# Kernel tuning notes

Hardware: AMD Instinct MI355X
Metric: run time of the kernel (lower is better)

The kernel has to match this reference:

```python
import jax, jax.numpy as jnp
import numpy as np

NOISE_SIGMA = 0.07
NOISE_TIMESTEPS = np.array([0, 1, 2, 3])
T, B, N_INP, N_REC, N_OUT = 256, 256, 128, 512, 64


def setup_inputs() -> dict:
    key = jax.random.key(0)
    ks = jax.random.split(key, 7)
    inputs = jax.random.normal(ks[0], (T, B, N_INP), dtype=jnp.float32)
    # Precomputed noise: randn*sigma at noise timesteps, zeros elsewhere
    noise = jnp.zeros((T, B, N_REC), dtype=jnp.float32)
    nz = jax.random.normal(ks[1], (len(NOISE_TIMESTEPS), B, N_REC), dtype=jnp.float32) * NOISE_SIGMA
    noise = noise.at[jnp.asarray(NOISE_TIMESTEPS)].set(nz)
    Wi = jax.random.normal(ks[2], (N_REC, N_INP), dtype=jnp.float32) / np.sqrt(N_INP)
    bi = jax.random.normal(ks[3], (N_REC,), dtype=jnp.float32) * 0.01
    # orthogonal recurrent init
    A = jax.random.normal(ks[4], (N_REC, N_REC), dtype=jnp.float32)
    Q, _ = jnp.linalg.qr(A)
    Wrec = Q.astype(jnp.float32)
    Wo = jax.random.normal(ks[5], (N_OUT, N_REC), dtype=jnp.float32) / np.sqrt(N_REC)
    bo = jax.random.normal(ks[6], (N_OUT,), dtype=jnp.float32) * 0.01
    return {"inputs": inputs, "noise": noise, "Wi": Wi, "bi": bi,
            "Wrec": Wrec, "Wo": Wo, "bo": bo}


def reference(inputs, noise, Wi, bi, Wrec, Wo, bo):
    # Precompute input projection for all timesteps: [T, B, n_rec]
    proj = jnp.einsum('tbi,ri->tbr', inputs, Wi) + bi

    def step(hidden, xs):
        p, nz = xs
        hidden = jax.nn.relu(p + hidden @ Wrec.T + nz)  # [B, n_rec]
        return hidden, hidden

    h0 = jnp.zeros((inputs.shape[1], Wrec.shape[0]), dtype=inputs.dtype)
    hidden, h = jax.lax.scan(step, h0, (proj, noise))
    output = jax.nn.softmax(hidden @ Wo.T + bo, axis=-1)  # [B, n_out]
    return output, h, hidden
```

## Files before the change

kernel.cpp:

```cpp
#include <hip/hip_runtime.h>
#include <hip/hip_bf16.h>
#include <stdint.h>

#define T_STEPS 256
#define B_SZ    256
#define NI      128
#define NR      512
#define NO      64
#define BT      16
#define HALF_R  256

typedef __attribute__((ext_vector_type(8))) short short8;
typedef __attribute__((ext_vector_type(4))) short short4v;
typedef __attribute__((ext_vector_type(4))) float f32x4;
typedef __attribute__((ext_vector_type(2))) unsigned long long u64x2;

__device__ __forceinline__ unsigned short f2bf(float f) {
    union { float f; unsigned u; } v; v.f = f;
    unsigned u = v.u;
    return (unsigned short)((u + 0x7FFFu + ((u >> 16) & 1u)) >> 16);
}

template<int KTB>
__device__ __forceinline__ void recur8(const unsigned char* Hbuf,
                                       const short8 (&Bh)[2][16],
                                       f32x4& acc0, f32x4& acc1,
                                       int l15, int l4, unsigned swzA) {
    #pragma unroll
    for (int kk = 0; kk < 8; ++kk) {
        const unsigned off = l15 * 1024 + (((unsigned)((KTB + kk) * 64 + l4 * 16)) ^ swzA);
        const short8 a = *(const short8*)(Hbuf + off);
        acc0 = __builtin_amdgcn_mfma_f32_16x16x32_bf16(a, Bh[0][KTB + kk], acc0, 0, 0, 0);
        acc1 = __builtin_amdgcn_mfma_f32_16x16x32_bf16(a, Bh[1][KTB + kk], acc1, 0, 0, 0);
    }
}

__global__ __launch_bounds__(256) void proj_gemm(
    const float* __restrict__ inputs, const float* __restrict__ Wi,
    const float* __restrict__ bi, const float* __restrict__ noise,
    float* __restrict__ proj)
{
    const int mb = blockIdx.x;
    const int nb = blockIdx.y;
    const int m0 = mb * 64, n0 = nb * 128;
    const int tid = threadIdx.x, w = tid >> 6, l = tid & 63;
    const int l15 = l & 15, l4 = l >> 4;

    __shared__ __align__(16) unsigned char Al[64 * 256];
    __shared__ __align__(16) unsigned char Wl[128 * 256];

    #pragma unroll
    for (int j = 0; j < 8; ++j) {
        const int f = j * 256 + tid;
        const int row = f >> 5, c4 = f & 31;
        const float4 v = *(const float4*)(inputs + (size_t)(m0 + row) * NI + c4 * 4);
        short4v pk;
        pk[0] = (short)f2bf(v.x); pk[1] = (short)f2bf(v.y);
        pk[2] = (short)f2bf(v.z); pk[3] = (short)f2bf(v.w);
        *(short4v*)(&Al[row * 256 + (((unsigned)(c4 * 8)) ^ ((row & 7) << 4))]) = pk;
    }
    #pragma unroll
    for (int j = 0; j < 16; ++j) {
        const int f = j * 256 + tid;
        const int r = f >> 5, c4 = f & 31;
        const float4 v = *(const float4*)(Wi + (size_t)(n0 + r) * NI + c4 * 4);
        short4v pk;
        pk[0] = (short)f2bf(v.x); pk[1] = (short)f2bf(v.y);
        pk[2] = (short)f2bf(v.z); pk[3] = (short)f2bf(v.w);
        *(short4v*)(&Wl[r * 256 + (((unsigned)(c4 * 8)) ^ ((r & 7) << 4))]) = pk;
    }
    __syncthreads();

    f32x4 acc[8];
    #pragma unroll
    for (int nt = 0; nt < 8; ++nt) acc[nt] = (f32x4){0.f, 0.f, 0.f, 0.f};
    #pragma unroll
    for (int kt = 0; kt < 4; ++kt) {
        const short8 a = *(const short8*)(
            &Al[(w * 16 + l15) * 256 + (((unsigned)(kt * 64 + l4 * 16)) ^ ((l15 & 7) << 4))]);
        #pragma unroll
        for (int nt = 0; nt < 8; ++nt) {
            const short8 b = *(const short8*)(
                &Wl[(nt * 16 + l15) * 256 + (((unsigned)(kt * 64 + l4 * 16)) ^ ((l15 & 7) << 4))]);
            acc[nt] = __builtin_amdgcn_mfma_f32_16x16x32_bf16(a, b, acc[nt], 0, 0, 0);
        }
    }

    const int t = m0 >> 8;
    #pragma unroll
    for (int nt = 0; nt < 8; ++nt) {
        const int n = n0 + nt * 16 + l15;
        const float bv = bi[n];
        #pragma unroll
        for (int q = 0; q < 4; ++q) {
            const int gr = m0 + w * 16 + l4 * 4 + q;
            float v = acc[nt][q] + bv;
            if (t < 4) v += noise[(size_t)gr * NR + n];
            proj[(size_t)gr * NR + n] = v;
        }
    }
}

__global__ __launch_bounds__(512) void rnn_scan(
    const float* __restrict__ Wrec,
    float* __restrict__ dout,
    unsigned long long* __restrict__ Xbuf)
{
    const int bid  = blockIdx.x;
    const int grp  = bid & 15;
    const int half = bid >> 4;
    const int b0   = grp * BT;
    const int tid  = threadIdx.x;
    const int w    = tid >> 6;
    const int l    = tid & 63;
    const int l15  = l & 15;
    const int l4   = l >> 4;

    __shared__ __align__(16) unsigned char Hl[2][BT * 1024];

    short8 Bh[2][16];
    #pragma unroll
    for (int ct = 0; ct < 2; ++ct) {
        const int n = half * HALF_R + w * 32 + ct * 16 + l15;
        #pragma unroll
        for (int kt = 0; kt < 16; ++kt) {
            const float* src = Wrec + (size_t)n * NR + kt * 32 + l4 * 8;
            short8 f;
            #pragma unroll
            for (int j = 0; j < 8; ++j) f[j] = (short)f2bf(src[j]);
            Bh[ct][kt] = f;
        }
    }

    unsigned long long* Xg = Xbuf + (size_t)grp * 4096;

    float* hbuf   = dout + (size_t)NO * B_SZ;
    float* hidout = hbuf + (size_t)T_STEPS * B_SZ * NR;

    const unsigned swzA = (unsigned)((l15 & 7) << 4);
    const int n0 = half * HALF_R + w * 32 + l15;
    const int n1 = n0 + 16;
    const int mrow = l4 * 4;

    f32x4 acc0, acc1;
    #pragma unroll
    for (int q = 0; q < 4; ++q) {
        acc0[q] = hbuf[(size_t)(b0 + mrow + q) * NR + n0];
        acc1[q] = hbuf[(size_t)(b0 + mrow + q) * NR + n1];
    }

    float pj0[4], pj1[4];

    for (int t = 0; t < T_STEPS; ++t) {
        const int pn = (t & 1) ^ 1;
        const int tag = ((t >> 1) & 1) ^ 1;

        if (t > 0) {
            if (half == 0) recur8<8>(&Hl[t & 1][0], Bh, acc0, acc1, l15, l4, swzA);
            else           recur8<0>(&Hl[t & 1][0], Bh, acc0, acc1, l15, l4, swzA);
        }

        float v0[4], v1[4];
        #pragma unroll
        for (int q = 0; q < 4; ++q) {
            v0[q] = fmaxf(acc0[q], 0.f);
            v1[q] = fmaxf(acc1[q], 0.f);
        }

        if (t == T_STEPS - 1) {
            #pragma unroll
            for (int q = 0; q < 4; ++q) {
                hbuf[((size_t)t * B_SZ + b0 + mrow + q) * NR + n0] = v0[q];
                hbuf[((size_t)t * B_SZ + b0 + mrow + q) * NR + n1] = v1[q];
                hidout[(size_t)(b0 + mrow + q) * NR + n0] = v0[q];
                hidout[(size_t)(b0 + mrow + q) * NR + n1] = v1[q];
            }
            break;
        }

        {
            unsigned long long* Xh = Xg + (size_t)(pn * 2 + half) * 1024;
            const unsigned long long tagmask =
                tag ? 0x8000800080008000ULL : 0ULL;
            #pragma unroll
            for (int ct = 0; ct < 2; ++ct) {
                #pragma unroll
                for (int q = 0; q < 4; ++q) {
                    const float v = ct ? v1[q] : v0[q];
                    const float vo = __shfl_xor(v, 1, 64);
                    unsigned pk = (unsigned)f2bf(v) | ((unsigned)f2bf(vo) << 16);
                    const unsigned pk_hi = __shfl_xor(pk, 2, 64);
                    if ((l & 3) == 0) {
                        const int m = mrow + q;
                        const int c = w * 32 + ct * 16 + l15;
                        const unsigned long long val =
                            (unsigned long long)pk | ((unsigned long long)pk_hi << 32);
                        const unsigned off = m * 1024 +
                            (((unsigned)(2 * (half * HALF_R + c))) ^ ((unsigned)((m & 7) << 4)));
                        *(unsigned long long*)(&Hl[pn][off]) = val;
                        __hip_atomic_store(Xh + m * 64 + (c >> 2), val | tagmask,
                                           __ATOMIC_RELAXED, __HIP_MEMORY_SCOPE_AGENT);
                    }
                }
            }
        }

        asm volatile("s_waitcnt lgkmcnt(0)" ::: "memory");
        __builtin_amdgcn_sched_barrier(0);
        __builtin_amdgcn_s_barrier();
        __builtin_amdgcn_sched_barrier(0);

        #pragma unroll
        for (int q = 0; q < 4; ++q) {
            pj0[q] = hbuf[((size_t)(t + 1) * B_SZ + b0 + mrow + q) * NR + n0];
            pj1[q] = hbuf[((size_t)(t + 1) * B_SZ + b0 + mrow + q) * NR + n1];
        }
        #pragma unroll
        for (int q = 0; q < 4; ++q) {
            hbuf[((size_t)t * B_SZ + b0 + mrow + q) * NR + n0] = v0[q];
            hbuf[((size_t)t * B_SZ + b0 + mrow + q) * NR + n1] = v1[q];
        }
        acc0 = (f32x4){0.f, 0.f, 0.f, 0.f};
        acc1 = (f32x4){0.f, 0.f, 0.f, 0.f};
        if (half == 0) recur8<0>(&Hl[pn][0], Bh, acc0, acc1, l15, l4, swzA);
        else           recur8<8>(&Hl[pn][0], Bh, acc0, acc1, l15, l4, swzA);

        {
            const int row = tid >> 5;
            const unsigned kk = (unsigned)((2 * tid) & 63);
            const unsigned long long* src =
                Xg + (size_t)(pn * 2 + (half ^ 1)) * 1024 + row * 64 + kk;
            const unsigned et = (unsigned)tag;
            unsigned long long a, b;
            for (;;) {
                a = __hip_atomic_load(src,     __ATOMIC_RELAXED, __HIP_MEMORY_SCOPE_AGENT);
                b = __hip_atomic_load(src + 1, __ATOMIC_RELAXED, __HIP_MEMORY_SCOPE_AGENT);
                if ((((unsigned)(a >> 63)) == et) & (((unsigned)(b >> 63)) == et)) break;
            }
            if (tag) { a &= 0x7FFF7FFF7FFF7FFFULL; b &= 0x7FFF7FFF7FFF7FFFULL; }
            u64x2 dd; dd[0] = a; dd[1] = b;
            const unsigned off = row * 1024 +
                (((unsigned)((half ^ 1) * 512 + kk * 8)) ^ ((unsigned)((row & 7) << 4)));
            *(u64x2*)(&Hl[pn][off]) = dd;
        }
        #pragma unroll
        for (int q = 0; q < 4; ++q) { acc0[q] += pj0[q]; acc1[q] += pj1[q]; }

        asm volatile("s_waitcnt lgkmcnt(0)" ::: "memory");
        __builtin_amdgcn_sched_barrier(0);
        __builtin_amdgcn_s_barrier();
        __builtin_amdgcn_sched_barrier(0);
    }
}

__global__ __launch_bounds__(256) void rnn_out(
    const float* __restrict__ Wo, const float* __restrict__ bo,
    float* __restrict__ dout)
{
    const float* hidden = dout + (size_t)NO * B_SZ + (size_t)T_STEPS * B_SZ * NR;
    const int b = blockIdx.x;
    const int tid = threadIdx.x, w = tid >> 6, l = tid & 63;

    __shared__ float hid[NR];
    __shared__ float lg[NO];

    if (tid < 128) {
        *(float4*)(&hid[tid * 4]) = *(const float4*)(hidden + (size_t)b * NR + tid * 4);
    }
    __syncthreads();

    #pragma unroll 1
    for (int jj = 0; jj < 16; ++jj) {
        const int j = w * 16 + jj;
        const float4* wr = (const float4*)(Wo + (size_t)j * NR + l * 8);
        const float4 a = wr[0], c = wr[1];
        const float4 h0 = *(const float4*)(&hid[l * 8]);
        const float4 h1 = *(const float4*)(&hid[l * 8 + 4]);
        float s = a.x * h0.x + a.y * h0.y + a.z * h0.z + a.w * h0.w
                + c.x * h1.x + c.y * h1.y + c.z * h1.z + c.w * h1.w;
        #pragma unroll
        for (int d = 32; d > 0; d >>= 1) s += __shfl_xor(s, d, 64);
        if (l == 0) lg[j] = s + bo[j];
    }
    __syncthreads();

    if (tid < 64) {
        const float x = lg[tid];
        float mx = x;
        #pragma unroll
        for (int d = 32; d > 0; d >>= 1) mx = fmaxf(mx, __shfl_xor(mx, d, 64));
        const float e = __expf(x - mx);
        float sum = e;
        #pragma unroll
        for (int d = 32; d > 0; d >>= 1) sum += __shfl_xor(sum, d, 64);
        dout[(size_t)b * NO + tid] = e / sum;
    }
}

extern "C" void kernel_launch(void* const* d_in, const int* in_sizes, int n_in,
                              void* d_out, int out_size, void* d_ws, size_t ws_size,
                              hipStream_t stream) {
    const float* inputs = (const float*)d_in[0];
    const float* noise  = (const float*)d_in[1];
    const float* Wi     = (const float*)d_in[2];
    const float* bi     = (const float*)d_in[3];
    const float* Wrec   = (const float*)d_in[4];
    const float* Wo     = (const float*)d_in[5];
    const float* bo     = (const float*)d_in[6];
    float* out = (float*)d_out;

    unsigned long long* Xbuf = (unsigned long long*)d_ws;

    float* proj = out + (size_t)NO * B_SZ;

    hipMemsetAsync(d_ws, 0, 16 * 4096 * sizeof(unsigned long long), stream);
    proj_gemm<<<dim3(1024, 4), 256, 0, stream>>>(inputs, Wi, bi, noise, proj);
    rnn_scan<<<32, 512, 0, stream>>>(Wrec, out, Xbuf);
    rnn_out<<<256, 256, 0, stream>>>(Wo, bo, out);
}
```

Measured before the change: 683.6 us.

## Split recurrent matmul by K across block pairs, exchange fp32 partial sums

```diff
diff --git a/kernel.cpp b/kernel.cpp
--- a/kernel.cpp
+++ b/kernel.cpp
@@ -13,7 +13,6 @@
 typedef __attribute__((ext_vector_type(8))) short short8;
 typedef __attribute__((ext_vector_type(4))) short short4v;
 typedef __attribute__((ext_vector_type(4))) float f32x4;
-typedef __attribute__((ext_vector_type(2))) unsigned long long u64x2;
 
 __device__ __forceinline__ unsigned short f2bf(float f) {
     union { float f; unsigned u; } v; v.f = f;
@@ -21,18 +20,10 @@
     return (unsigned short)((u + 0x7FFFu + ((u >> 16) & 1u)) >> 16);
 }
 
-template<int KTB>
-__device__ __forceinline__ void recur8(const unsigned char* Hbuf,
-                                       const short8 (&Bh)[2][16],
-                                       f32x4& acc0, f32x4& acc1,
-                                       int l15, int l4, unsigned swzA) {
-    #pragma unroll
-    for (int kk = 0; kk < 8; ++kk) {
-        const unsigned off = l15 * 1024 + (((unsigned)((KTB + kk) * 64 + l4 * 16)) ^ swzA);
-        const short8 a = *(const short8*)(Hbuf + off);
-        acc0 = __builtin_amdgcn_mfma_f32_16x16x32_bf16(a, Bh[0][KTB + kk], acc0, 0, 0, 0);
-        acc1 = __builtin_amdgcn_mfma_f32_16x16x32_bf16(a, Bh[1][KTB + kk], acc1, 0, 0, 0);
-    }
+__device__ __forceinline__ unsigned long long tagpack2(float a, float b, unsigned tag) {
+    const unsigned ua = (__float_as_uint(a) & ~1u) | tag;
+    const unsigned ub = (__float_as_uint(b) & ~1u) | tag;
+    return (unsigned long long)ua | ((unsigned long long)ub << 32);
 }
 
 __global__ __launch_bounds__(256) void proj_gemm(
@@ -101,7 +92,7 @@
     }
 }
 
-__global__ __launch_bounds__(512) void rnn_scan(
+__global__ __launch_bounds__(512, 2) void rnn_scan(
     const float* __restrict__ Wrec,
     float* __restrict__ dout,
     unsigned long long* __restrict__ Xbuf)
@@ -115,16 +106,20 @@
     const int l    = tid & 63;
     const int l15  = l & 15;
     const int l4   = l >> 4;
-
-    __shared__ __align__(16) unsigned char Hl[2][BT * 1024];
-
-    short8 Bh[2][16];
-    #pragma unroll
-    for (int ct = 0; ct < 2; ++ct) {
-        const int n = half * HALF_R + w * 32 + ct * 16 + l15;
-        #pragma unroll
-        for (int kt = 0; kt < 16; ++kt) {
-            const float* src = Wrec + (size_t)n * NR + kt * 32 + l4 * 8;
+    const bool keep = ((w >> 2) == half);
+    const int kw   = w & 3;
+    const int mrow = l4 * 4;
+    const int nb   = w * 64;
+
+    __shared__ __align__(16) unsigned char Hl[2][BT * 512];
+
+    short8 Bh[4][8];
+    #pragma unroll
+    for (int ct = 0; ct < 4; ++ct) {
+        const int n = nb + ct * 16 + l15;
+        #pragma unroll
+        for (int kt = 0; kt < 8; ++kt) {
+            const float* src = Wrec + (size_t)n * NR + half * HALF_R + kt * 32 + l4 * 8;
             short8 f;
             #pragma unroll
             for (int j = 0; j < 8; ++j) f[j] = (short)f2bf(src[j]);
@@ -132,119 +127,156 @@
         }
     }
 
-    unsigned long long* Xg = Xbuf + (size_t)grp * 4096;
+    unsigned long long* Xg = Xbuf + (size_t)grp * 8192;
 
     float* hbuf   = dout + (size_t)NO * B_SZ;
     float* hidout = hbuf + (size_t)T_STEPS * B_SZ * NR;
 
-    const unsigned swzA = (unsigned)((l15 & 7) << 4);
-    const int n0 = half * HALF_R + w * 32 + l15;
-    const int n1 = n0 + 16;
-    const int mrow = l4 * 4;
-
-    f32x4 acc0, acc1;
-    #pragma unroll
-    for (int q = 0; q < 4; ++q) {
-        acc0[q] = hbuf[(size_t)(b0 + mrow + q) * NR + n0];
-        acc1[q] = hbuf[(size_t)(b0 + mrow + q) * NR + n1];
-    }
-
-    float pj0[4], pj1[4];
-
-    for (int t = 0; t < T_STEPS; ++t) {
-        const int pn = (t & 1) ^ 1;
-        const int tag = ((t >> 1) & 1) ^ 1;
-
-        if (t > 0) {
-            if (half == 0) recur8<8>(&Hl[t & 1][0], Bh, acc0, acc1, l15, l4, swzA);
-            else           recur8<0>(&Hl[t & 1][0], Bh, acc0, acc1, l15, l4, swzA);
-        }
-
-        float v0[4], v1[4];
-        #pragma unroll
-        for (int q = 0; q < 4; ++q) {
-            v0[q] = fmaxf(acc0[q], 0.f);
-            v1[q] = fmaxf(acc1[q], 0.f);
-        }
-
-        if (t == T_STEPS - 1) {
+    float pj[4][4];
+
+    if (keep) {
+        #pragma unroll
+        for (int ct = 0; ct < 4; ++ct)
+            #pragma unroll
+            for (int q = 0; q < 4; ++q)
+                pj[ct][q] = hbuf[(size_t)(b0 + mrow + q) * NR + nb + ct * 16 + l15];
+        #pragma unroll
+        for (int ct = 0; ct < 4; ++ct) {
             #pragma unroll
             for (int q = 0; q < 4; ++q) {
-                hbuf[((size_t)t * B_SZ + b0 + mrow + q) * NR + n0] = v0[q];
-                hbuf[((size_t)t * B_SZ + b0 + mrow + q) * NR + n1] = v1[q];
-                hidout[(size_t)(b0 + mrow + q) * NR + n0] = v0[q];
-                hidout[(size_t)(b0 + mrow + q) * NR + n1] = v1[q];
-            }
-            break;
-        }
-
-        {
-            unsigned long long* Xh = Xg + (size_t)(pn * 2 + half) * 1024;
-            const unsigned long long tagmask =
-                tag ? 0x8000800080008000ULL : 0ULL;
-            #pragma unroll
-            for (int ct = 0; ct < 2; ++ct) {
+                const float v = fmaxf(pj[ct][q], 0.f);
+                hbuf[(size_t)(b0 + mrow + q) * NR + nb + ct * 16 + l15] = v;
+                const float vo = __shfl_xor(v, 1, 64);
+                unsigned pk = (unsigned)f2bf(v) | ((unsigned)f2bf(vo) << 16);
+                const unsigned pk_hi = __shfl_xor(pk, 2, 64);
+                if ((l & 3) == 0) {
+                    const int c = kw * 64 + ct * 16 + l15;
+                    const int m = mrow + q;
+                    const unsigned off = m * 512 +
+                        (((unsigned)(2 * c)) ^ ((unsigned)((m & 7) << 4)));
+                    *(unsigned long long*)(&Hl[0][off]) =
+                        (unsigned long long)pk | ((unsigned long long)pk_hi << 32);
+                }
+            }
+        }
+        #pragma unroll
+        for (int ct = 0; ct < 4; ++ct)
+            #pragma unroll
+            for (int q = 0; q < 4; ++q)
+                pj[ct][q] = hbuf[((size_t)B_SZ + b0 + mrow + q) * NR + nb + ct * 16 + l15];
+    }
+    asm volatile("s_waitcnt lgkmcnt(0)" ::: "memory");
+    __builtin_amdgcn_sched_barrier(0);
+    __builtin_amdgcn_s_barrier();
+    __builtin_amdgcn_sched_barrier(0);
+
+    for (int t = 1; t < T_STEPS; ++t) {
+        const int p = t & 1;
+        const unsigned tag = ((unsigned)(t + 1) >> 1) & 1u;
+        const unsigned char* Hb = &Hl[p ^ 1][0];
+
+        f32x4 acc[4];
+        #pragma unroll
+        for (int ct = 0; ct < 4; ++ct) acc[ct] = (f32x4){0.f, 0.f, 0.f, 0.f};
+
+        unsigned long long* Xe =
+            Xg + (size_t)(p * 2 + (half ^ 1)) * 2048 + kw * 512 + l;
+
+        if (!keep) __builtin_amdgcn_s_setprio(1);
+        #pragma unroll
+        for (int ct = 0; ct < 4; ++ct) {
+            #pragma unroll
+            for (int kt = 0; kt < 8; ++kt) {
+                const unsigned off = l15 * 512 +
+                    (((unsigned)(kt * 64 + l4 * 16)) ^ ((unsigned)((l15 & 7) << 4)));
+                const short8 a = *(const short8*)(Hb + off);
+                acc[ct] = __builtin_amdgcn_mfma_f32_16x16x32_bf16(a, Bh[ct][kt], acc[ct], 0, 0, 0);
+            }
+            if (!keep) {
+                __hip_atomic_store(Xe + ct * 128,
+                                   tagpack2(acc[ct][0], acc[ct][1], tag),
+                                   __ATOMIC_RELAXED, __HIP_MEMORY_SCOPE_AGENT);
+                __hip_atomic_store(Xe + ct * 128 + 64,
+                                   tagpack2(acc[ct][2], acc[ct][3], tag),
+                                   __ATOMIC_RELAXED, __HIP_MEMORY_SCOPE_AGENT);
+            }
+        }
+        if (!keep) __builtin_amdgcn_s_setprio(0);
+
+        if (keep) {
+            const unsigned long long* Xc =
+                Xg + (size_t)(p * 2 + half) * 2048 + kw * 512 + l;
+            const unsigned long long tmask =
+                tag ? 0x0000000100000001ULL : 0ULL;
+            unsigned long long d0, d1, d2, d3, d4, d5, d6, d7;
+            for (;;) {
+                d0 = __hip_atomic_load(Xc +   0, __ATOMIC_RELAXED, __HIP_MEMORY_SCOPE_AGENT);
+                d1 = __hip_atomic_load(Xc +  64, __ATOMIC_RELAXED, __HIP_MEMORY_SCOPE_AGENT);
+                d2 = __hip_atomic_load(Xc + 128, __ATOMIC_RELAXED, __HIP_MEMORY_SCOPE_AGENT);
+                d3 = __hip_atomic_load(Xc + 192, __ATOMIC_RELAXED, __HIP_MEMORY_SCOPE_AGENT);
+                d4 = __hip_atomic_load(Xc + 256, __ATOMIC_RELAXED, __HIP_MEMORY_SCOPE_AGENT);
+                d5 = __hip_atomic_load(Xc + 320, __ATOMIC_RELAXED, __HIP_MEMORY_SCOPE_AGENT);
+                d6 = __hip_atomic_load(Xc + 384, __ATOMIC_RELAXED, __HIP_MEMORY_SCOPE_AGENT);
+                d7 = __hip_atomic_load(Xc + 448, __ATOMIC_RELAXED, __HIP_MEMORY_SCOPE_AGENT);
+                const unsigned long long bad =
+                    (((d0 ^ tmask) | (d1 ^ tmask) | (d2 ^ tmask) | (d3 ^ tmask) |
+                      (d4 ^ tmask) | (d5 ^ tmask) | (d6 ^ tmask) | (d7 ^ tmask))
+                     & 0x0000000100000001ULL);
+                if (bad == 0) break;
+            }
+
+            float vv[4][4];
+            #pragma unroll
+            for (int ct = 0; ct < 4; ++ct) {
+                const unsigned long long da = (ct == 0) ? d0 : (ct == 1) ? d2 : (ct == 2) ? d4 : d6;
+                const unsigned long long db = (ct == 0) ? d1 : (ct == 1) ? d3 : (ct == 2) ? d5 : d7;
+                vv[ct][0] = fmaxf(acc[ct][0] + __uint_as_float((unsigned)da)         + pj[ct][0], 0.f);
+                vv[ct][1] = fmaxf(acc[ct][1] + __uint_as_float((unsigned)(da >> 32)) + pj[ct][1], 0.f);
+                vv[ct][2] = fmaxf(acc[ct][2] + __uint_as_float((unsigned)db)         + pj[ct][2], 0.f);
+                vv[ct][3] = fmaxf(acc[ct][3] + __uint_as_float((unsigned)(db >> 32)) + pj[ct][3], 0.f);
+            }
+
+            #pragma unroll
+            for (int ct = 0; ct < 4; ++ct) {
                 #pragma unroll
                 for (int q = 0; q < 4; ++q) {
-                    const float v = ct ? v1[q] : v0[q];
+                    const float v = vv[ct][q];
                     const float vo = __shfl_xor(v, 1, 64);
                     unsigned pk = (unsigned)f2bf(v) | ((unsigned)f2bf(vo) << 16);
                     const unsigned pk_hi = __shfl_xor(pk, 2, 64);
                     if ((l & 3) == 0) {
+                        const int c = kw * 64 + ct * 16 + l15;
                         const int m = mrow + q;
-                        const int c = w * 32 + ct * 16 + l15;
-                        const unsigned long long val =
+                        const unsigned off = m * 512 +
+                            (((unsigned)(2 * c)) ^ ((unsigned)((m & 7) << 4)));
+                        *(unsigned long long*)(&Hl[p][off]) =
                             (unsigned long long)pk | ((unsigned long long)pk_hi << 32);
-                        const unsigned off = m * 1024 +
-                            (((unsigned)(2 * (half * HALF_R + c))) ^ ((unsigned)((m & 7) << 4)));
-                        *(unsigned long long*)(&Hl[pn][off]) = val;
-                        __hip_atomic_store(Xh + m * 64 + (c >> 2), val | tagmask,
-                                           __ATOMIC_RELAXED, __HIP_MEMORY_SCOPE_AGENT);
                     }
                 }
             }
-        }
-
-        asm volatile("s_waitcnt lgkmcnt(0)" ::: "memory");
-        __builtin_amdgcn_sched_barrier(0);
-        __builtin_amdgcn_s_barrier();
-        __builtin_amdgcn_sched_barrier(0);
-
-        #pragma unroll
-        for (int q = 0; q < 4; ++q) {
-            pj0[q] = hbuf[((size_t)(t + 1) * B_SZ + b0 + mrow + q) * NR + n0];
-            pj1[q] = hbuf[((size_t)(t + 1) * B_SZ + b0 + mrow + q) * NR + n1];
-        }
-        #pragma unroll
-        for (int q = 0; q < 4; ++q) {
-            hbuf[((size_t)t * B_SZ + b0 + mrow + q) * NR + n0] = v0[q];
-            hbuf[((size_t)t * B_SZ + b0 + mrow + q) * NR + n1] = v1[q];
-        }
-        acc0 = (f32x4){0.f, 0.f, 0.f, 0.f};
-        acc1 = (f32x4){0.f, 0.f, 0.f, 0.f};
-        if (half == 0) recur8<0>(&Hl[pn][0], Bh, acc0, acc1, l15, l4, swzA);
-        else           recur8<8>(&Hl[pn][0], Bh, acc0, acc1, l15, l4, swzA);
-
-        {
-            const int row = tid >> 5;
-            const unsigned kk = (unsigned)((2 * tid) & 63);
-            const unsigned long long* src =
-                Xg + (size_t)(pn * 2 + (half ^ 1)) * 1024 + row * 64 + kk;
-            const unsigned et = (unsigned)tag;
-            unsigned long long a, b;
-            for (;;) {
-                a = __hip_atomic_load(src,     __ATOMIC_RELAXED, __HIP_MEMORY_SCOPE_AGENT);
-                b = __hip_atomic_load(src + 1, __ATOMIC_RELAXED, __HIP_MEMORY_SCOPE_AGENT);
-                if ((((unsigned)(a >> 63)) == et) & (((unsigned)(b >> 63)) == et)) break;
-            }
-            if (tag) { a &= 0x7FFF7FFF7FFF7FFFULL; b &= 0x7FFF7FFF7FFF7FFFULL; }
-            u64x2 dd; dd[0] = a; dd[1] = b;
-            const unsigned off = row * 1024 +
-                (((unsigned)((half ^ 1) * 512 + kk * 8)) ^ ((unsigned)((row & 7) << 4)));
-            *(u64x2*)(&Hl[pn][off]) = dd;
-        }
-        #pragma unroll
-        for (int q = 0; q < 4; ++q) { acc0[q] += pj0[q]; acc1[q] += pj1[q]; }
+
+            if (t < T_STEPS - 1) {
+                #pragma unroll
+                for (int ct = 0; ct < 4; ++ct)
+                    #pragma unroll
+                    for (int q = 0; q < 4; ++q)
+                        hbuf[((size_t)t * B_SZ + b0 + mrow + q) * NR + nb + ct * 16 + l15] = vv[ct][q];
+                #pragma unroll
+                for (int ct = 0; ct < 4; ++ct)
+                    #pragma unroll
+                    for (int q = 0; q < 4; ++q)
+                        pj[ct][q] = hbuf[((size_t)(t + 1) * B_SZ + b0 + mrow + q) * NR + nb + ct * 16 + l15];
+            } else {
+                #pragma unroll
+                for (int ct = 0; ct < 4; ++ct) {
+                    #pragma unroll
+                    for (int q = 0; q < 4; ++q) {
+                        hbuf[((size_t)t * B_SZ + b0 + mrow + q) * NR + nb + ct * 16 + l15] = vv[ct][q];
+                        hidout[(size_t)(b0 + mrow + q) * NR + nb + ct * 16 + l15] = vv[ct][q];
+                    }
+                }
+            }
+        }
 
         asm volatile("s_waitcnt lgkmcnt(0)" ::: "memory");
         __builtin_amdgcn_sched_barrier(0);
@@ -313,7 +345,7 @@
 
     float* proj = out + (size_t)NO * B_SZ;
 
-    hipMemsetAsync(d_ws, 0, 16 * 4096 * sizeof(unsigned long long), stream);
+    (void)hipMemsetAsync(d_ws, 0, (size_t)16 * 8192 * sizeof(unsigned long long), stream);
     proj_gemm<<<dim3(1024, 4), 256, 0, stream>>>(inputs, Wi, bi, noise, proj);
     rnn_scan<<<32, 512, 0, stream>>>(Wrec, out, Xbuf);
     rnn_out<<<256, 256, 0, stream>>>(Wo, bo, out);
```

Result: slower. 1.221 ms (+78.6%).
